# Kernel tuning notes

Measured on AMD Instinct MI355X. Metric: run time of the kernel, lower is better.

## Reference

```python
import jax, jax.numpy as jnp
import numpy as np

B, S, E = 4, 2048, 768
H, D = 3, E // 3  # 3 heads of size emb_sz//3


def setup_inputs() -> dict:
    key = jax.random.key(0)
    ks = jax.random.split(key, 8)
    inp = {
        "inputs_for_keys": jax.random.normal(ks[0], (B, S, E), jnp.float32),
        "inputs_for_values": jax.random.normal(ks[1], (B, S, E), jnp.float32),
        "inputs_for_queries": jax.random.normal(ks[2], (B, S, E), jnp.float32),
        # stacked per-head projections: [H, E, D] (same math as 3 separate tensordots)
        "WK": jax.random.normal(ks[3], (H, E, D), jnp.float32) * 0.02,
        "WV": jax.random.normal(ks[4], (H, E, D), jnp.float32) * 0.02,
        "WQ": jax.random.normal(ks[5], (H, E, D), jnp.float32) * 0.02,
        "Wo": jax.random.normal(ks[6], (E, E), jnp.float32) * 0.02,
        "bo": jnp.zeros((E,), jnp.float32),
    }
    return inp


def reference(inputs_for_keys, inputs_for_values, inputs_for_queries, WK, WV, WQ, Wo, bo):
    # per-head projections: [B, H, S, D]
    K = jnp.einsum("bse,hed->bhsd", inputs_for_keys, WK)
    V = jnp.einsum("bse,hed->bhsd", inputs_for_values, WV)
    Q = jnp.einsum("bse,hed->bhsd", inputs_for_queries, WQ)

    Sk = K.shape[2]
    # NOTE: original scales by sqrt(window_size_keys), not sqrt(head_dim)
    scores = jnp.einsum("bhqd,bhkd->bhqk", Q, K) / np.sqrt(Sk).astype(np.float32)
    # strictly-upper-triangular -inf causal mask (use_mask=True)
    causal = jnp.tril(jnp.ones((Q.shape[2], Sk), dtype=bool))
    scores = jnp.where(causal, scores, -jnp.inf)

    probs = jax.nn.softmax(scores, axis=-1)
    Z = jnp.einsum("bhqk,bhkd->bhqd", probs, V)  # [B, H, S, D]
    # concat heads (order 1,2,3) -> [B, S, E]
    concat = Z.transpose(0, 2, 1, 3).reshape(Z.shape[0], Z.shape[2], -1)
    return concat @ Wo + bo
```

## Files before the change

### kernel.cpp

```cpp
#include <hip/hip_runtime.h>
#include <hip/hip_bf16.h>

#define Bq 4
#define Sq 2048
#define Eq 768
#define Hq 3
#define Dq 256
#define BHq (Bq*Hq)

typedef __hip_bfloat16 bf16;
typedef __attribute__((ext_vector_type(8))) short bf16x8;
typedef __attribute__((ext_vector_type(4))) float f32x4;

__device__ __forceinline__ f32x4 mfma16(bf16x8 a, bf16x8 b, f32x4 c) {
    return __builtin_amdgcn_mfma_f32_16x16x32_bf16(a, b, c, 0, 0, 0);
}

__device__ __forceinline__ short f2bf(float x) {
    bf16 b = __float2bfloat16(x);
    return *(short*)&b;
}

__device__ __forceinline__ float bf2f(short s) {
    bf16 b = *reinterpret_cast<bf16*>(&s);
    return __bfloat162float(b);
}

__device__ __forceinline__ bf16x8 cvt8(float4 a, float4 b) {
    bf16x8 r;
    r[0] = f2bf(a.x); r[1] = f2bf(a.y); r[2] = f2bf(a.z); r[3] = f2bf(a.w);
    r[4] = f2bf(b.x); r[5] = f2bf(b.y); r[6] = f2bf(b.z); r[7] = f2bf(b.w);
    return r;
}

__device__ __forceinline__ void gl2lds16(const bf16* g, bf16* l) {
    __builtin_amdgcn_global_load_lds(
        (const __attribute__((address_space(1))) unsigned int*)g,
        (__attribute__((address_space(3))) unsigned int*)l,
        16, 0, 0);
}

__global__ __launch_bounds__(256) void prep_kernel(
        const float* __restrict__ Xk, const float* __restrict__ Xv,
        const float* __restrict__ Xq, bf16* __restrict__ Xb,
        const float* __restrict__ WK, const float* __restrict__ WV,
        const float* __restrict__ WQ, const float* __restrict__ Wo,
        bf16* __restrict__ WtK, bf16* __restrict__ Wot) {
    const int blk = blockIdx.x;
    const int tid = threadIdx.x;

    if (blk < 9216) {
        const int t = blk / 3072;
        const int i = blk % 3072;
        const float* X = (t == 0) ? Xk : (t == 1) ? Xv : Xq;
        size_t idx = ((size_t)i * 256 + tid) * 8;
        float4 a = *(const float4*)&X[idx];
        float4 b = *(const float4*)&X[idx + 4];
        *(bf16x8*)&Xb[(size_t)t * ((size_t)Bq * Sq * Eq) + idx] = cvt8(a, b);
        return;
    }

    __shared__ float tile[32][33];
    const float* in;
    bf16* out;
    int R, C, bx, by;
    if (blk < 10944) {
        int r  = blk - 9216;
        int t  = r / 576;
        int rr = r % 576;
        int batch = rr / 192;
        int tl = rr % 192;
        bx = tl & 7; by = tl >> 3;
        R = Eq; C = Dq;
        const float* Wsrc = (t == 0) ? WK : (t == 1) ? WV : WQ;
        in  = Wsrc + (size_t)batch * R * C;
        out = WtK + (size_t)t * ((size_t)Hq * Eq * Dq) + (size_t)batch * R * C;
    } else {
        int rr = blk - 10944;
        bx = rr % 24; by = rr / 24;
        R = Eq; C = Eq;
        in  = Wo;
        out = Wot;
    }
    const int tx = tid & 31;
    const int ty = tid >> 5;
#pragma unroll
    for (int i = ty; i < 32; i += 8)
        tile[i][tx] = in[(size_t)(by * 32 + i) * C + bx * 32 + tx];
    __syncthreads();
#pragma unroll
    for (int i = ty; i < 32; i += 8)
        out[(size_t)(bx * 32 + i) * R + by * 32 + tx] = __float2bfloat16(tile[tx][i]);
}

__global__ __launch_bounds__(256) void proj_kernel(
        const bf16* __restrict__ Xb, const bf16* __restrict__ Wt,
        bf16* __restrict__ Kp, bf16* __restrict__ Vt, bf16* __restrict__ Qp) {
    const int sel = blockIdx.y;
    const int x   = blockIdx.x;
    const int xcd = x & 7;
    const int kk0 = x >> 3;
    const int mt  = xcd * 8 + (kk0 / 6);
    const int nt  = kk0 % 6;
    const bf16* X = Xb + (size_t)sel * ((size_t)Bq * Sq * Eq);
    const bf16* W = Wt + (size_t)sel * ((size_t)Hq * Eq * Dq);

    __shared__ struct {
        bf16 A[2][128 * 32];
        bf16 B[2][128 * 32];
    } sm;
    auto& As = sm.A;
    auto& Bs = sm.B;

    const int tid  = threadIdx.x;
    const int lane = tid & 63;
    const int w    = tid >> 6;
    const int quad = lane >> 4;
    const int l16  = lane & 15;
    const int wm   = (w & 1) * 64;
    const int wn   = (w >> 1) * 64;

    const int m0 = mt * 128;
    const int n0 = nt * 128;

    int srow[2], skc[2];
#pragma unroll
    for (int i = 0; i < 2; ++i) {
        int ci  = (w * 2 + i) * 64 + lane;
        srow[i] = ci >> 2;
        skc[i]  = (ci & 3) ^ ((srow[i] >> 1) & 3);
    }

#define STAGE(buf, k0)                                                        \
    {                                                                         \
        _Pragma("unroll")                                                     \
        for (int i = 0; i < 2; ++i) {                                         \
            gl2lds16(&X[(size_t)(m0 + srow[i]) * Eq + (k0) + skc[i] * 8],     \
                     &As[buf][(w * 2 + i) * 512]);                            \
            gl2lds16(&W[(size_t)(n0 + srow[i]) * Eq + (k0) + skc[i] * 8],     \
                     &Bs[buf][(w * 2 + i) * 512]);                            \
        }                                                                     \
    }

    STAGE(0, 0);
    __syncthreads();

    f32x4 acc[4][4] = {};

    for (int s = 0; s < 24; ++s) {
        if (s + 1 < 24) STAGE((s + 1) & 1, (s + 1) * 32);
        const bf16* A  = As[s & 1];
        const bf16* Bv = Bs[s & 1];
        bf16x8 af[4], bfr[4];
#pragma unroll
        for (int mi = 0; mi < 4; ++mi) {
            int row = wm + mi * 16 + l16;
            int c   = quad ^ ((row >> 1) & 3);
            af[mi]  = *(const bf16x8*)&A[row * 32 + c * 8];
        }
#pragma unroll
        for (int ni = 0; ni < 4; ++ni) {
            int row = wn + ni * 16 + l16;
            int c   = quad ^ ((row >> 1) & 3);
            bfr[ni] = *(const bf16x8*)&Bv[row * 32 + c * 8];
        }
#pragma unroll
        for (int mi = 0; mi < 4; ++mi)
#pragma unroll
            for (int ni = 0; ni < 4; ++ni)
                acc[mi][ni] = mfma16(af[mi], bfr[ni], acc[mi][ni]);
        __syncthreads();
    }
#undef STAGE

    bf16* ct = (bf16*)&sm;
    const int b  = m0 / Sq;
    const int s0 = m0 % Sq;
    const int h  = n0 >> 8;
    const int d0 = n0 & 255;
    const int bh = b * Hq + h;

    if (sel == 1) {
#pragma unroll
        for (int mi = 0; mi < 4; ++mi)
#pragma unroll
            for (int ni = 0; ni < 4; ++ni)
#pragma unroll
                for (int r = 0; r < 4; ++r) {
                    int row = wn + ni * 16 + l16;
                    int col = wm + mi * 16 + quad * 4 + r;
                    ct[row * 128 + (((col >> 3) ^ (row & 15)) * 8) + (col & 7)] =
                        __float2bfloat16(acc[mi][ni][r]);
                }
    } else {
#pragma unroll
        for (int mi = 0; mi < 4; ++mi)
#pragma unroll
            for (int ni = 0; ni < 4; ++ni)
#pragma unroll
                for (int r = 0; r < 4; ++r) {
                    int row = wm + mi * 16 + quad * 4 + r;
                    int col = wn + ni * 16 + l16;
                    ct[row * 128 + (((col >> 3) ^ (row & 15)) * 8) + (col & 7)] =
                        __float2bfloat16(acc[mi][ni][r]);
                }
    }
    __syncthreads();
    {
        const int rr = tid >> 4;
        const int c  = tid & 15;
#pragma unroll
        for (int p = 0; p < 8; ++p) {
            int r  = p * 16 + rr;
            int cp = c ^ (r & 15);
            bf16x8 v = *(const bf16x8*)&ct[r * 128 + cp * 8];
            if (sel == 1)
                *(bf16x8*)&Vt[(size_t)(bh * Dq + d0 + r) * Sq + s0 + c * 8] = v;
            else if (sel == 0)
                *(bf16x8*)&Kp[(size_t)(bh * Sq + s0 + r) * Dq + d0 + c * 8] = v;
            else
                *(bf16x8*)&Qp[(size_t)(bh * Sq + s0 + r) * Dq + d0 + c * 8] = v;
        }
    }
}

__global__ __launch_bounds__(256, 2) void attn_kernel(
        const bf16* __restrict__ Qp, const bf16* __restrict__ Kp,
        const bf16* __restrict__ Vt, bf16* __restrict__ Z,
        bf16* __restrict__ Opart, float* __restrict__ lpart) {
    __shared__ bf16 Ks[64 * 256];
    __shared__ bf16 Vs[256 * 64];
    __shared__ bf16 Pl[4 * 16 * 64];

    const float SCALE = 0.022097086912079608f;

    const int id    = blockIdx.x;
    const int lane8 = id & 7;
    const int j     = id >> 3;
    const int W     = lane8 * 216 + j;
    const int bh    = W / 144;
    const int w144  = W % 144;
    int g = 0;
#pragma unroll
    for (int gg = 1; gg < 8; ++gg)
        if (w144 >= 2 * gg * (gg + 1)) g = gg;
    const int rem   = w144 - 2 * g * (g + 1);
    const int qb    = g * 4 + rem / (g + 1);
    const int chunk = rem % (g + 1);
    const int t0    = chunk * 4;
    const int t1    = min(t0 + 4, qb + 1);
    const bool single = (qb < 4);

    const int tid  = threadIdx.x;
    const int lane = tid & 63;
    const int w    = tid >> 6;
    const int quad = lane >> 4;
    const int l16  = lane & 15;
    const int q0   = qb * 64 + w * 16;

    bf16x8 qf[8];
    {
        const bf16* Qbase = Qp + (size_t)(bh * Sq + q0 + l16) * Dq;
#pragma unroll
        for (int c = 0; c < 8; ++c)
            qf[c] = *(const bf16x8*)&Qbase[c * 32 + quad * 8];
    }

    const bf16* Kbh = Kp + (size_t)bh * Sq * Dq;
    const bf16* Vbh = Vt + (size_t)bh * Dq * Sq;

    f32x4 o[16] = {};
    float lsum[4] = {0.0f, 0.0f, 0.0f, 0.0f};

    for (int t = t0; t < t1; ++t) {
        const int k0 = t * 64;

        bf16x8 kreg[8], vreg[8];
#pragma unroll
        for (int p = 0; p < 8; ++p) {
            int c = p * 256 + tid;
            int row = c >> 5, cc = c & 31;
            kreg[p] = *(const bf16x8*)&Kbh[(size_t)(k0 + row) * Dq + cc * 8];
        }
#pragma unroll
        for (int p = 0; p < 8; ++p) {
            int c = p * 256 + tid;
            int row = c >> 3, cc = c & 7;
            vreg[p] = *(const bf16x8*)&Vbh[(size_t)row * Sq + k0 + cc * 8];
        }

        __syncthreads();
#pragma unroll
        for (int p = 0; p < 8; ++p) {
            int c = p * 256 + tid;
            int row = c >> 5, cc = c & 31;
            *(bf16x8*)&Ks[row * 256 + (cc ^ (row & 7)) * 8] = kreg[p];
        }
#pragma unroll
        for (int p = 0; p < 8; ++p) {
            int c = p * 256 + tid;
            int row = c >> 3, cc = c & 7;
            *(bf16x8*)&Vs[row * 64 + (cc ^ (row & 7)) * 8] = vreg[p];
        }
        __syncthreads();

        f32x4 sf[4] = {};
#pragma unroll
        for (int c = 0; c < 8; ++c) {
            int cc = c * 4 + quad;
#pragma unroll
            for (int ni = 0; ni < 4; ++ni) {
                int key = ni * 16 + l16;
                bf16x8 kf = *(const bf16x8*)&Ks[key * 256 + (cc ^ (key & 7)) * 8];
                sf[ni] = mfma16(qf[c], kf, sf[ni]);
            }
        }

        const bool diag = (t == qb);
        float pv[4][4];
#pragma unroll
        for (int ni = 0; ni < 4; ++ni) {
#pragma unroll
            for (int r = 0; r < 4; ++r) {
                float p = __expf(sf[ni][r] * SCALE);
                if (diag) {
                    int kg = k0 + ni * 16 + l16;
                    int qg = q0 + quad * 4 + r;
                    if (kg > qg) p = 0.0f;
                }
                pv[ni][r] = p;
                lsum[r] += p;
            }
        }

#pragma unroll
        for (int ni = 0; ni < 4; ++ni) {
#pragma unroll
            for (int r = 0; r < 4; ++r) {
                int row = quad * 4 + r;
                int col = ni * 16 + l16;
                int cc  = col >> 3;
                Pl[w * 1024 + row * 64 + (cc ^ (row & 7)) * 8 + (col & 7)] =
                    __float2bfloat16(pv[ni][r]);
            }
        }

#pragma unroll
        for (int c2 = 0; c2 < 2; ++c2) {
            int cc = c2 * 4 + quad;
            bf16x8 af = *(const bf16x8*)&Pl[w * 1024 + l16 * 64 + (cc ^ (l16 & 7)) * 8];
#pragma unroll
            for (int ni = 0; ni < 16; ++ni) {
                int d = ni * 16 + l16;
                bf16x8 vf = *(const bf16x8*)&Vs[d * 64 + (cc ^ (d & 7)) * 8];
                o[ni] = mfma16(af, vf, o[ni]);
            }
        }
    }

#pragma unroll
    for (int off = 1; off < 16; off <<= 1)
#pragma unroll
        for (int r = 0; r < 4; ++r)
            lsum[r] += __shfl_xor(lsum[r], off);

    if (single) {
        const int b = bh / Hq, h = bh % Hq;
        float rinv[4];
#pragma unroll
        for (int r = 0; r < 4; ++r) rinv[r] = 1.0f / lsum[r];
#pragma unroll
        for (int ni = 0; ni < 16; ++ni) {
#pragma unroll
            for (int r = 0; r < 4; ++r) {
                int s = q0 + quad * 4 + r;
                int e = h * Dq + ni * 16 + l16;
                Z[(size_t)(b * Sq + s) * Eq + e] = __float2bfloat16(o[ni][r] * rinv[r]);
            }
        }
    } else {
        const int slot = bh * 144 + w144;
        bf16* Ob = Opart + (size_t)slot * (64 * 256);
#pragma unroll
        for (int ni = 0; ni < 16; ++ni) {
#pragma unroll
            for (int r = 0; r < 4; ++r) {
                int row = w * 16 + quad * 4 + r;
                int col = ni * 16 + l16;
                Ob[row * 256 + col] = __float2bfloat16(o[ni][r]);
            }
        }
        if (l16 == 0) {
#pragma unroll
            for (int r = 0; r < 4; ++r)
                lpart[(size_t)slot * 64 + w * 16 + quad * 4 + r] = lsum[r];
        }
    }
}

__global__ __launch_bounds__(256) void combine_kernel(
        const bf16* __restrict__ Opart, const float* __restrict__ lpart,
        bf16* __restrict__ Z) {
    const int qb = blockIdx.x;
    const int bh = blockIdx.y;
    if (qb < 4) return;
    const int g = qb >> 2;
    const int nch = g + 1;
    const int wbase = 2 * g * (g + 1) + (qb & 3) * (g + 1);
    const int slot0 = bh * 144 + wbase;

    const int tid = threadIdx.x;
    const int r   = tid >> 2;
    const int cs  = tid & 3;

    float l = 0.0f;
    for (int c = 0; c < nch; ++c)
        l += lpart[(size_t)(slot0 + c) * 64 + r];
    const float rinv = 1.0f / l;

    const int b = bh / Hq, h = bh % Hq;
    const int s = qb * 64 + r;
    bf16* zrow = Z + (size_t)(b * Sq + s) * Eq + h * Dq;

#pragma unroll
    for (int seg = 0; seg < 8; ++seg) {
        int col0 = cs * 64 + seg * 8;
        float acc[8] = {};
        for (int c = 0; c < nch; ++c) {
            bf16x8 v = *(const bf16x8*)&Opart[(size_t)(slot0 + c) * (64 * 256) + r * 256 + col0];
#pragma unroll
            for (int i = 0; i < 8; ++i) {
                short sv = v[i];
                acc[i] += bf2f(sv);
            }
        }
        bf16x8 outv;
#pragma unroll
        for (int i = 0; i < 8; ++i) outv[i] = f2bf(acc[i] * rinv);
        *(bf16x8*)&zrow[col0] = outv;
    }
}

__global__ __launch_bounds__(256) void outproj_kernel(
        const bf16* __restrict__ Z, const bf16* __restrict__ Wot,
        const float* __restrict__ bo, float* __restrict__ out) {
    const int x   = blockIdx.x;
    const int xcd = x & 7;
    const int kk0 = x >> 3;
    const int mt  = xcd * 8 + (kk0 / 6);
    const int nt  = kk0 % 6;

    __shared__ bf16 As[2][128 * 32];
    __shared__ bf16 Bs[2][128 * 32];

    const int tid  = threadIdx.x;
    const int lane = tid & 63;
    const int w    = tid >> 6;
    const int quad = lane >> 4;
    const int l16  = lane & 15;
    const int wm   = (w & 1) * 64;
    const int wn   = (w >> 1) * 64;

    const int m0 = mt * 128;
    const int n0 = nt * 128;

    int srow[2], skc[2];
#pragma unroll
    for (int i = 0; i < 2; ++i) {
        int ci  = (w * 2 + i) * 64 + lane;
        srow[i] = ci >> 2;
        skc[i]  = (ci & 3) ^ ((srow[i] >> 1) & 3);
    }

#define STAGE2(buf, k0)                                                       \
    {                                                                         \
        _Pragma("unroll")                                                     \
        for (int i = 0; i < 2; ++i) {                                         \
            gl2lds16(&Z[(size_t)(m0 + srow[i]) * Eq + (k0) + skc[i] * 8],     \
                     &As[buf][(w * 2 + i) * 512]);                            \
            gl2lds16(&Wot[(size_t)(n0 + srow[i]) * Eq + (k0) + skc[i] * 8],   \
                     &Bs[buf][(w * 2 + i) * 512]);                            \
        }                                                                     \
    }

    STAGE2(0, 0);
    __syncthreads();

    f32x4 acc[4][4] = {};

    for (int s = 0; s < 24; ++s) {
        if (s + 1 < 24) STAGE2((s + 1) & 1, (s + 1) * 32);
        const bf16* A  = As[s & 1];
        const bf16* Bv = Bs[s & 1];
        bf16x8 af[4], bfr[4];
#pragma unroll
        for (int mi = 0; mi < 4; ++mi) {
            int row = wm + mi * 16 + l16;
            int c   = quad ^ ((row >> 1) & 3);
            af[mi]  = *(const bf16x8*)&A[row * 32 + c * 8];
        }
#pragma unroll
        for (int ni = 0; ni < 4; ++ni) {
            int row = wn + ni * 16 + l16;
            int c   = quad ^ ((row >> 1) & 3);
            bfr[ni] = *(const bf16x8*)&Bv[row * 32 + c * 8];
        }
#pragma unroll
        for (int mi = 0; mi < 4; ++mi)
#pragma unroll
            for (int ni = 0; ni < 4; ++ni)
                acc[mi][ni] = mfma16(af[mi], bfr[ni], acc[mi][ni]);
        __syncthreads();
    }
#undef STAGE2

#pragma unroll
    for (int ni = 0; ni < 4; ++ni) {
        int n = n0 + wn + ni * 16 + l16;
        float bias = bo[n];
#pragma unroll
        for (int mi = 0; mi < 4; ++mi) {
#pragma unroll
            for (int r = 0; r < 4; ++r) {
                int m = m0 + wm + mi * 16 + quad * 4 + r;
                out[(size_t)m * Eq + n] = acc[mi][ni][r] + bias;
            }
        }
    }
}

extern "C" void kernel_launch(void* const* d_in, const int* in_sizes, int n_in,
                              void* d_out, int out_size, void* d_ws, size_t ws_size,
                              hipStream_t stream) {
    const float* Xk = (const float*)d_in[0];
    const float* Xv = (const float*)d_in[1];
    const float* Xq = (const float*)d_in[2];
    const float* WK = (const float*)d_in[3];
    const float* WV = (const float*)d_in[4];
    const float* WQ = (const float*)d_in[5];
    const float* Wo = (const float*)d_in[6];
    const float* bo = (const float*)d_in[7];
    float* out = (float*)d_out;

    bf16* ws = (bf16*)d_ws;
    const size_t WSZ  = (size_t)Hq * Eq * Dq;
    const size_t QKV  = (size_t)BHq * Sq * Dq;
    bf16* WtK = ws;
    bf16* WtO = WtK + 3 * WSZ;
    bf16* Qp  = WtO + (size_t)Eq * Eq;
    bf16* Kp  = Qp + QKV;
    bf16* Vt  = Kp + QKV;
    bf16* Zb  = Vt + QKV;
    bf16* Opart = Zb + QKV;
    float* lpart = (float*)(Opart + (size_t)1728 * 64 * 256);
    bf16* Xb = Opart;

    prep_kernel<<<11520, 256, 0, stream>>>(Xk, Xv, Xq, Xb, WK, WV, WQ, Wo, WtK, WtO);
    proj_kernel<<<dim3(384, 3), 256, 0, stream>>>(Xb, WtK, Kp, Vt, Qp);
    attn_kernel<<<1728, 256, 0, stream>>>(Qp, Kp, Vt, Zb, Opart, lpart);
    combine_kernel<<<dim3(32, BHq), 256, 0, stream>>>(Opart, lpart, Zb);
    outproj_kernel<<<384, 256, 0, stream>>>(Zb, WtO, bo, out);
}
```

Before: 320.9 us.

## Restructure attention PV split, async K staging, and drop V shared-memory tile

Each wave now computes the P·V product for all 64 query rows but only a 64-wide slice of the head dimension. It reads its V fragments directly from global memory into registers, so the V shared-memory tile is gone. K tiles are staged asynchronously with direct global-to-LDS loads and prefetched for the next iteration during the PV MFMAs. MFMA sections get raised priority, occupancy is raised to 3 blocks per CU, and P is shared through a padded LDS buffer. The cost is extra barriers and cross-wave row-sum exchange in the epilogue, and the gl2lds16 helper is not visible in the diff.

```diff
diff --git a/kernel.cpp b/kernel.cpp
--- a/kernel.cpp
+++ b/kernel.cpp
@@ -224,13 +224,12 @@
     }
 }
 
-__global__ __launch_bounds__(256, 2) void attn_kernel(
+__global__ __launch_bounds__(256, 3) void attn_kernel(
         const bf16* __restrict__ Qp, const bf16* __restrict__ Kp,
         const bf16* __restrict__ Vt, bf16* __restrict__ Z,
         bf16* __restrict__ Opart, float* __restrict__ lpart) {
     __shared__ bf16 Ks[64 * 256];
-    __shared__ bf16 Vs[256 * 64];
-    __shared__ bf16 Pl[4 * 16 * 64];
+    __shared__ bf16 Pl[64 * 72];
 
     const float SCALE = 0.022097086912079608f;
 
@@ -269,55 +268,50 @@
     const bf16* Kbh = Kp + (size_t)bh * Sq * Dq;
     const bf16* Vbh = Vt + (size_t)bh * Dq * Sq;
 
-    f32x4 o[16] = {};
+#define STAGEK(k0)                                                            \
+    {                                                                         \
+        _Pragma("unroll")                                                     \
+        for (int p = 0; p < 8; ++p) {                                         \
+            int c   = p * 256 + tid;                                          \
+            int row = c >> 5, cc = c & 31;                                    \
+            gl2lds16(&Kbh[(size_t)((k0) + row) * Dq + ((cc ^ (row & 7)) * 8)],\
+                     &Ks[(p * 256 + w * 64) * 8]);                            \
+        }                                                                     \
+    }
+
+    f32x4 o[4][4] = {};
     float lsum[4] = {0.0f, 0.0f, 0.0f, 0.0f};
+
+    STAGEK(t0 * 64);
 
     for (int t = t0; t < t1; ++t) {
         const int k0 = t * 64;
 
-        bf16x8 kreg[8], vreg[8];
-#pragma unroll
-        for (int p = 0; p < 8; ++p) {
-            int c = p * 256 + tid;
-            int row = c >> 5, cc = c & 31;
-            kreg[p] = *(const bf16x8*)&Kbh[(size_t)(k0 + row) * Dq + cc * 8];
-        }
-#pragma unroll
-        for (int p = 0; p < 8; ++p) {
-            int c = p * 256 + tid;
-            int row = c >> 3, cc = c & 7;
-            vreg[p] = *(const bf16x8*)&Vbh[(size_t)row * Sq + k0 + cc * 8];
-        }
-
-        __syncthreads();
-#pragma unroll
-        for (int p = 0; p < 8; ++p) {
-            int c = p * 256 + tid;
-            int row = c >> 5, cc = c & 31;
-            *(bf16x8*)&Ks[row * 256 + (cc ^ (row & 7)) * 8] = kreg[p];
-        }
-#pragma unroll
-        for (int p = 0; p < 8; ++p) {
-            int c = p * 256 + tid;
-            int row = c >> 3, cc = c & 7;
-            *(bf16x8*)&Vs[row * 64 + (cc ^ (row & 7)) * 8] = vreg[p];
-        }
-        __syncthreads();
+        asm volatile("s_waitcnt vmcnt(0)" ::: "memory");
+        bf16x8 vreg[4][2];
+#pragma unroll
+        for (int ni = 0; ni < 4; ++ni)
+#pragma unroll
+            for (int kk = 0; kk < 2; ++kk)
+                vreg[ni][kk] = *(const bf16x8*)&Vbh[
+                    (size_t)(w * 64 + ni * 16 + l16) * Sq + k0 + kk * 32 + quad * 8];
+        __builtin_amdgcn_s_barrier();
 
         f32x4 sf[4] = {};
+        __builtin_amdgcn_s_setprio(1);
 #pragma unroll
         for (int c = 0; c < 8; ++c) {
             int cc = c * 4 + quad;
 #pragma unroll
             for (int ni = 0; ni < 4; ++ni) {
                 int key = ni * 16 + l16;
-                bf16x8 kf = *(const bf16x8*)&Ks[key * 256 + (cc ^ (key & 7)) * 8];
+                bf16x8 kf = *(const bf16x8*)&Ks[key * 256 + ((cc ^ (key & 7)) * 8)];
                 sf[ni] = mfma16(qf[c], kf, sf[ni]);
             }
         }
+        __builtin_amdgcn_s_setprio(0);
 
         const bool diag = (t == qb);
-        float pv[4][4];
 #pragma unroll
         for (int ni = 0; ni < 4; ++ni) {
 #pragma unroll
@@ -328,35 +322,30 @@
                     int qg = q0 + quad * 4 + r;
                     if (kg > qg) p = 0.0f;
                 }
-                pv[ni][r] = p;
                 lsum[r] += p;
+                Pl[(w * 16 + quad * 4 + r) * 72 + ni * 16 + l16] =
+                    __float2bfloat16(p);
             }
         }
 
-#pragma unroll
-        for (int ni = 0; ni < 4; ++ni) {
-#pragma unroll
-            for (int r = 0; r < 4; ++r) {
-                int row = quad * 4 + r;
-                int col = ni * 16 + l16;
-                int cc  = col >> 3;
-                Pl[w * 1024 + row * 64 + (cc ^ (row & 7)) * 8 + (col & 7)] =
-                    __float2bfloat16(pv[ni][r]);
+        __syncthreads();
+
+        if (t + 1 < t1) STAGEK(k0 + 64);
+
+        __builtin_amdgcn_s_setprio(1);
+#pragma unroll
+        for (int mi = 0; mi < 4; ++mi) {
+            bf16x8 af0 = *(const bf16x8*)&Pl[(mi * 16 + l16) * 72 + quad * 8];
+            bf16x8 af1 = *(const bf16x8*)&Pl[(mi * 16 + l16) * 72 + 32 + quad * 8];
+#pragma unroll
+            for (int ni = 0; ni < 4; ++ni) {
+                o[mi][ni] = mfma16(af0, vreg[ni][0], o[mi][ni]);
+                o[mi][ni] = mfma16(af1, vreg[ni][1], o[mi][ni]);
             }
         }
-
-#pragma unroll
-        for (int c2 = 0; c2 < 2; ++c2) {
-            int cc = c2 * 4 + quad;
-            bf16x8 af = *(const bf16x8*)&Pl[w * 1024 + l16 * 64 + (cc ^ (l16 & 7)) * 8];
-#pragma unroll
-            for (int ni = 0; ni < 16; ++ni) {
-                int d = ni * 16 + l16;
-                bf16x8 vf = *(const bf16x8*)&Vs[d * 64 + (cc ^ (d & 7)) * 8];
-                o[ni] = mfma16(af, vf, o[ni]);
-            }
-        }
-    }
+        __builtin_amdgcn_s_setprio(0);
+    }
+#undef STAGEK
 
 #pragma unroll
     for (int off = 1; off < 16; off <<= 1)
@@ -365,31 +354,46 @@
             lsum[r] += __shfl_xor(lsum[r], off);
 
     if (single) {
+        float* ls = (float*)Pl;
+        __syncthreads();
+        if (l16 == 0) {
+#pragma unroll
+            for (int r = 0; r < 4; ++r)
+                ls[w * 16 + quad * 4 + r] = lsum[r];
+        }
+        __syncthreads();
+
         const int b = bh / Hq, h = bh % Hq;
-        float rinv[4];
-#pragma unroll
-        for (int r = 0; r < 4; ++r) rinv[r] = 1.0f / lsum[r];
-#pragma unroll
-        for (int ni = 0; ni < 16; ++ni) {
-#pragma unroll
-            for (int r = 0; r < 4; ++r) {
-                int s = q0 + quad * 4 + r;
-                int e = h * Dq + ni * 16 + l16;
-                Z[(size_t)(b * Sq + s) * Eq + e] = __float2bfloat16(o[ni][r] * rinv[r]);
+#pragma unroll
+        for (int mi = 0; mi < 4; ++mi) {
+            float rinv[4];
+#pragma unroll
+            for (int r = 0; r < 4; ++r)
+                rinv[r] = 1.0f / ls[mi * 16 + quad * 4 + r];
+#pragma unroll
+            for (int ni = 0; ni < 4; ++ni) {
+#pragma unroll
+                for (int r = 0; r < 4; ++r) {
+                    int s = qb * 64 + mi * 16 + quad * 4 + r;
+                    int e = h * Dq + w * 64 + ni * 16 + l16;
+                    Z[(size_t)(b * Sq + s) * Eq + e] =
+                        __float2bfloat16(o[mi][ni][r] * rinv[r]);
+                }
             }
         }
     } else {
         const int slot = bh * 144 + w144;
         bf16* Ob = Opart + (size_t)slot * (64 * 256);
 #pragma unroll
-        for (int ni = 0; ni < 16; ++ni) {
-#pragma unroll
-            for (int r = 0; r < 4; ++r) {
-                int row = w * 16 + quad * 4 + r;
-                int col = ni * 16 + l16;
-                Ob[row * 256 + col] = __float2bfloat16(o[ni][r]);
-            }
-        }
+        for (int mi = 0; mi < 4; ++mi)
+#pragma unroll
+            for (int ni = 0; ni < 4; ++ni)
+#pragma unroll
+                for (int r = 0; r < 4; ++r) {
+                    int row = mi * 16 + quad * 4 + r;
+                    int col = w * 64 + ni * 16 + l16;
+                    Ob[row * 256 + col] = __float2bfloat16(o[mi][ni][r]);
+                }
         if (l16 == 0) {
 #pragma unroll
             for (int r = 0; r < 4; ++r)
```

New measurement: 373.7 us. +16.5%, slower.

## Double attention query tile to 128 rows with 512-thread blocks sharing K/V tiles

Applied to the files above, without the earlier changes.

Each attention block now covers 128 query rows with 8 waves (512 threads) instead of 64 rows with 4 waves, so every K/V tile loaded into shared memory serves twice as many queries and global K/V traffic halves. The work decomposition, partial-output slots and combine kernel are reworked for 128-row query blocks and chunks of up to 4 key tiles. The causal mask is now evaluated on every tile rather than only the diagonal, and the P store is fused into the exp loop. The risks are fewer blocks (864), a larger block that must fit 4 per CU under the launch bounds (register pressure from o[16]), and extra per-element mask compares.

```diff
diff --git a/kernel.cpp b/kernel.cpp
--- a/kernel.cpp
+++ b/kernel.cpp
@@ -224,39 +224,54 @@
     }
 }
 
-__global__ __launch_bounds__(256, 2) void attn_kernel(
+__global__ __launch_bounds__(512, 4) void attn_kernel(
         const bf16* __restrict__ Qp, const bf16* __restrict__ Kp,
         const bf16* __restrict__ Vt, bf16* __restrict__ Z,
         bf16* __restrict__ Opart, float* __restrict__ lpart) {
     __shared__ bf16 Ks[64 * 256];
     __shared__ bf16 Vs[256 * 64];
-    __shared__ bf16 Pl[4 * 16 * 64];
+    __shared__ bf16 Pl[8 * 16 * 64];
 
     const float SCALE = 0.022097086912079608f;
 
     const int id    = blockIdx.x;
     const int lane8 = id & 7;
     const int j     = id >> 3;
-    const int W     = lane8 * 216 + j;
-    const int bh    = W / 144;
-    const int w144  = W % 144;
-    int g = 0;
-#pragma unroll
-    for (int gg = 1; gg < 8; ++gg)
-        if (w144 >= 2 * gg * (gg + 1)) g = gg;
-    const int rem   = w144 - 2 * g * (g + 1);
-    const int qb    = g * 4 + rem / (g + 1);
-    const int chunk = rem % (g + 1);
+    const int W     = lane8 * 108 + j;
+    const int bh    = W / 72;
+    const int w72   = W % 72;
+    int qb = 0;
+    {
+        const int S1=1,S2=2,S3=4,S4=6,S5=9,S6=12,S7=16,S8=20,S9=25,S10=30,
+                  S11=36,S12=42,S13=49,S14=56,S15=64;
+        if (w72 >= S1)  qb = 1;
+        if (w72 >= S2)  qb = 2;
+        if (w72 >= S3)  qb = 3;
+        if (w72 >= S4)  qb = 4;
+        if (w72 >= S5)  qb = 5;
+        if (w72 >= S6)  qb = 6;
+        if (w72 >= S7)  qb = 7;
+        if (w72 >= S8)  qb = 8;
+        if (w72 >= S9)  qb = 9;
+        if (w72 >= S10) qb = 10;
+        if (w72 >= S11) qb = 11;
+        if (w72 >= S12) qb = 12;
+        if (w72 >= S13) qb = 13;
+        if (w72 >= S14) qb = 14;
+        if (w72 >= S15) qb = 15;
+    }
+    const int Sarr[16] = {0,1,2,4,6,9,12,16,20,25,30,36,42,49,56,64};
+    const int chunk = w72 - Sarr[qb];
     const int t0    = chunk * 4;
-    const int t1    = min(t0 + 4, qb + 1);
-    const bool single = (qb < 4);
+    const int t1    = min(t0 + 4, 2 * qb + 2);
+    const bool single = (qb < 2);
 
     const int tid  = threadIdx.x;
     const int lane = tid & 63;
     const int w    = tid >> 6;
     const int quad = lane >> 4;
     const int l16  = lane & 15;
-    const int q0   = qb * 64 + w * 16;
+    const int q0   = qb * 128 + w * 16;
 
     bf16x8 qf[8];
     {
@@ -275,30 +290,30 @@
     for (int t = t0; t < t1; ++t) {
         const int k0 = t * 64;
 
-        bf16x8 kreg[8], vreg[8];
-#pragma unroll
-        for (int p = 0; p < 8; ++p) {
-            int c = p * 256 + tid;
+        bf16x8 kreg[4], vreg[4];
+#pragma unroll
+        for (int p = 0; p < 4; ++p) {
+            int c = p * 512 + tid;
             int row = c >> 5, cc = c & 31;
             kreg[p] = *(const bf16x8*)&Kbh[(size_t)(k0 + row) * Dq + cc * 8];
         }
 #pragma unroll
-        for (int p = 0; p < 8; ++p) {
-            int c = p * 256 + tid;
+        for (int p = 0; p < 4; ++p) {
+            int c = p * 512 + tid;
             int row = c >> 3, cc = c & 7;
             vreg[p] = *(const bf16x8*)&Vbh[(size_t)row * Sq + k0 + cc * 8];
         }
 
         __syncthreads();
 #pragma unroll
-        for (int p = 0; p < 8; ++p) {
-            int c = p * 256 + tid;
+        for (int p = 0; p < 4; ++p) {
+            int c = p * 512 + tid;
             int row = c >> 5, cc = c & 31;
             *(bf16x8*)&Ks[row * 256 + (cc ^ (row & 7)) * 8] = kreg[p];
         }
 #pragma unroll
-        for (int p = 0; p < 8; ++p) {
-            int c = p * 256 + tid;
+        for (int p = 0; p < 4; ++p) {
+            int c = p * 512 + tid;
             int row = c >> 3, cc = c & 7;
             *(bf16x8*)&Vs[row * 64 + (cc ^ (row & 7)) * 8] = vreg[p];
         }
@@ -316,32 +331,20 @@
             }
         }
 
-        const bool diag = (t == qb);
-        float pv[4][4];
 #pragma unroll
         for (int ni = 0; ni < 4; ++ni) {
 #pragma unroll
             for (int r = 0; r < 4; ++r) {
                 float p = __expf(sf[ni][r] * SCALE);
-                if (diag) {
-                    int kg = k0 + ni * 16 + l16;
-                    int qg = q0 + quad * 4 + r;
-                    if (kg > qg) p = 0.0f;
-                }
-                pv[ni][r] = p;
+                int kg = k0 + ni * 16 + l16;
+                int qg = q0 + quad * 4 + r;
+                if (kg > qg) p = 0.0f;
                 lsum[r] += p;
-            }
-        }
-
-#pragma unroll
-        for (int ni = 0; ni < 4; ++ni) {
-#pragma unroll
-            for (int r = 0; r < 4; ++r) {
                 int row = quad * 4 + r;
                 int col = ni * 16 + l16;
                 int cc  = col >> 3;
                 Pl[w * 1024 + row * 64 + (cc ^ (row & 7)) * 8 + (col & 7)] =
-                    __float2bfloat16(pv[ni][r]);
+                    __float2bfloat16(p);
             }
         }
 
@@ -379,8 +382,8 @@
             }
         }
     } else {
-        const int slot = bh * 144 + w144;
-        bf16* Ob = Opart + (size_t)slot * (64 * 256);
+        const int slot = bh * 72 + w72;
+        bf16* Ob = Opart + (size_t)slot * (128 * 256);
 #pragma unroll
         for (int ni = 0; ni < 16; ++ni) {
 #pragma unroll
@@ -393,7 +396,7 @@
         if (l16 == 0) {
 #pragma unroll
             for (int r = 0; r < 4; ++r)
-                lpart[(size_t)slot * 64 + w * 16 + quad * 4 + r] = lsum[r];
+                lpart[(size_t)slot * 128 + w * 16 + quad * 4 + r] = lsum[r];
         }
     }
 }
@@ -403,31 +406,30 @@
         bf16* __restrict__ Z) {
     const int qb = blockIdx.x;
     const int bh = blockIdx.y;
-    if (qb < 4) return;
-    const int g = qb >> 2;
-    const int nch = g + 1;
-    const int wbase = 2 * g * (g + 1) + (qb & 3) * (g + 1);
-    const int slot0 = bh * 144 + wbase;
+    if (qb < 2) return;
+    const int Sarr[16] = {0,1,2,4,6,9,12,16,20,25,30,36,42,49,56,64};
+    const int nch   = (qb + 2) >> 1;
+    const int slot0 = bh * 72 + Sarr[qb];
 
     const int tid = threadIdx.x;
-    const int r   = tid >> 2;
-    const int cs  = tid & 3;
+    const int r   = tid >> 1;
+    const int cs  = tid & 1;
 
     float l = 0.0f;
     for (int c = 0; c < nch; ++c)
-        l += lpart[(size_t)(slot0 + c) * 64 + r];
+        l += lpart[(size_t)(slot0 + c) * 128 + r];
     const float rinv = 1.0f / l;
 
     const int b = bh / Hq, h = bh % Hq;
-    const int s = qb * 64 + r;
+    const int s = qb * 128 + r;
     bf16* zrow = Z + (size_t)(b * Sq + s) * Eq + h * Dq;
 
 #pragma unroll
-    for (int seg = 0; seg < 8; ++seg) {
-        int col0 = cs * 64 + seg * 8;
+    for (int seg = 0; seg < 16; ++seg) {
+        int col0 = cs * 128 + seg * 8;
         float acc[8] = {};
         for (int c = 0; c < nch; ++c) {
-            bf16x8 v = *(const bf16x8*)&Opart[(size_t)(slot0 + c) * (64 * 256) + r * 256 + col0];
+            bf16x8 v = *(const bf16x8*)&Opart[(size_t)(slot0 + c) * (128 * 256) + r * 256 + col0];
 #pragma unroll
             for (int i = 0; i < 8; ++i) {
                 short sv = v[i];
@@ -552,12 +554,12 @@
     bf16* Vt  = Kp + QKV;
     bf16* Zb  = Vt + QKV;
     bf16* Opart = Zb + QKV;
-    float* lpart = (float*)(Opart + (size_t)1728 * 64 * 256);
+    float* lpart = (float*)(Opart + (size_t)864 * 128 * 256);
     bf16* Xb = Opart;
 
     prep_kernel<<<11520, 256, 0, stream>>>(Xk, Xv, Xq, Xb, WK, WV, WQ, Wo, WtK, WtO);
     proj_kernel<<<dim3(384, 3), 256, 0, stream>>>(Xb, WtK, Kp, Vt, Qp);
-    attn_kernel<<<1728, 256, 0, stream>>>(Qp, Kp, Vt, Zb, Opart, lpart);
-    combine_kernel<<<dim3(32, BHq), 256, 0, stream>>>(Opart, lpart, Zb);
+    attn_kernel<<<864, 512, 0, stream>>>(Qp, Kp, Vt, Zb, Opart, lpart);
+    combine_kernel<<<dim3(16, BHq), 256, 0, stream>>>(Opart, lpart, Zb);
     outproj_kernel<<<384, 256, 0, stream>>>(Zb, WtO, bo, out);
 }
```

New measurement: 394.7 us. 23.0% more time.
